# Kernel tuning notes

Hardware: AMD Instinct MI355X
Metric: run time of the kernel (lower is better)

Reference implementation:

```python
import jax, jax.numpy as jnp
import numpy as np

MAXDISP = 192  # must match init_kwargs max_disp


def _interp_axis(x, axis, out_size):
    """1-D linear interpolation along `axis` with align_corners=True."""
    in_size = x.shape[axis]
    src = jnp.arange(out_size, dtype=jnp.float32) * ((in_size - 1) / (out_size - 1))
    i0 = jnp.clip(jnp.floor(src).astype(jnp.int32), 0, in_size - 1)
    i1 = jnp.clip(i0 + 1, 0, in_size - 1)
    w = (src - i0.astype(jnp.float32)).astype(x.dtype)
    shape = [1] * x.ndim
    shape[axis] = out_size
    w = w.reshape(shape)
    return jnp.take(x, i0, axis=axis) * (1 - w) + jnp.take(x, i1, axis=axis) * w


def create_cost_volume(left, right, maxdisp):
    """Vectorized version of the original per-disparity slice-copy loop.
    cost[:, :C, d, :, w] = left[:, :, :, w]        if w >= d else 0
    cost[:, C:, d, :, w] = right[:, :, :, w - d]   if w >= d else 0
    Returns [B, 2C, D, H, W] with D = maxdisp // 4.
    """
    B, C, H, W = left.shape
    D = maxdisp // 4
    d = jnp.arange(D)[:, None]          # [D,1]
    w = jnp.arange(W)[None, :]          # [1,W]
    mask = (w >= d).astype(left.dtype)  # [D,W]
    idx = jnp.clip(w - d, 0, W - 1)     # [D,W] shifted gather indices
    mask_b = mask[None, None, :, None, :]                       # [1,1,D,1,W]
    cost_left = left[:, :, None, :, :] * mask_b                 # [B,C,D,H,W]
    cost_right = jnp.take(right, idx.reshape(-1), axis=3)       # [B,C,H,D*W]
    cost_right = cost_right.reshape(B, C, H, D, W)
    cost_right = jnp.transpose(cost_right, (0, 1, 3, 2, 4)) * mask_b
    return jnp.concatenate([cost_left, cost_right], axis=1)     # [B,2C,D,H,W]


def upsample_regression(vol, maxdisp):
    """Trilinear x4 upsample (align_corners=True) + softmax over disparity +
    soft-argmin expectation. vol: [B, D/4, H/4, W/4] -> [B, H, W]."""
    x = vol
    for axis in (1, 2, 3):
        x = _interp_axis(x, axis, x.shape[axis] * 4)
    p = jax.nn.softmax(x, axis=1)                       # [B, maxdisp, H, W]
    disps = jnp.arange(maxdisp, dtype=x.dtype)
    return jnp.einsum('bdhw,d->bhw', p, disps)


def setup_inputs() -> dict:
    key = jax.random.key(0)
    k1, k2 = jax.random.split(key)
    left = jax.random.normal(k1, (2, 32, 64, 128), dtype=jnp.float32)
    right = jax.random.normal(k2, (2, 32, 64, 128), dtype=jnp.float32)
    return {"left": left, "right": right}


def reference(left, right):
    cost = create_cost_volume(left, right, MAXDISP)  # [B,2C,D,H,W]
    # Stand-in for the (unavailable) stacked hourglass 3D-CNN: channel mean
    # reduces the cost volume to a single-channel disparity volume [B,D,H,W].
    vol = cost.mean(axis=1)
    return upsample_regression(vol, MAXDISP)  # [B, 4H, 4W]
```

## Files before the change

### kernel.cpp

```cpp
#include <hip/hip_runtime.h>

#define BB 2
#define CC 32
#define HC 64
#define WC 128
#define DC 48
#define HO 256
#define WO 512
#define MAXD 192

__global__ __launch_bounds__(256) void sum_channels_kernel(
    const float* __restrict__ left, const float* __restrict__ right,
    float* __restrict__ Ls, float* __restrict__ Rs) {
    __shared__ float sbuf[2][WC];
    int blk = blockIdx.x;
    int m   = blk >> 7;
    int b   = (blk >> 6) & 1;
    int h   = blk & (HC - 1);
    int t   = threadIdx.x;
    int sel = t >> 7;
    int w   = t & (WC - 1);

    const float* src = (m ? right : left)
                     + (size_t)b * (CC * HC * WC)
                     + (size_t)(sel * 16) * (HC * WC) + h * WC + w;
    float s = 0.f;
#pragma unroll
    for (int c = 0; c < 16; ++c) s += src[c * (HC * WC)];
    sbuf[sel][w] = s;
    __syncthreads();
    if (t < WC) {
        float* dst = m ? Rs : Ls;
        dst[b * (HC * WC) + h * WC + t] = sbuf[0][t] + sbuf[1][t];
    }
}

template <int K>
__device__ inline void quarter_work(const float* __restrict__ Rh,
                                    int w0, int w1, float c0, float c1,
                                    float lw0, float lw1,
                                    float& plsum, float& pssum) {
    constexpr int DDLO = 48 * K;
    constexpr int DDHI = 48 * K + 47;
    constexpr int DLO  = (DDLO * (DC - 1)) / (MAXD - 1);
    constexpr int DHI  = (DDHI * (DC - 1)) / (MAXD - 1);
    constexpr int NV   = DHI - DLO + 2;

    float vv[NV];
#pragma unroll
    for (int j = 0; j < NV; ++j) {
        int d = DLO + j;
        if (d > DC - 1) { vv[j] = vv[j - 1]; continue; }
        int i0 = w0 - d; float m0 = (i0 >= 0) ? 1.f : 0.f; i0 = max(i0, 0);
        int i1 = w1 - d; float m1 = (i1 >= 0) ? 1.f : 0.f; i1 = max(i1, 0);
        vv[j] = m0 * c0 * (lw0 + Rh[i0]) + m1 * c1 * (lw1 + Rh[i1]);
    }
    float ls = 0.f, ss = 0.f;
#pragma unroll
    for (int dd = DDLO; dd <= DDHI; ++dd) {
        int d    = (dd * (DC - 1)) / (MAXD - 1);
        float wd = (float)dd * (47.0f / 191.0f) - (float)d;
        float vc = vv[d - DLO];
        float x  = vc + wd * (vv[d - DLO + 1] - vc);
        float e  = __expf(x);
        ls += e;
        ss += e * (float)dd;
    }
    plsum = ls;
    pssum = ss;
}

__global__ __launch_bounds__(512) void disparity_kernel(
    const float* __restrict__ Ls, const float* __restrict__ Rs,
    float* __restrict__ out) {
    __shared__ float Lh[WC];
    __shared__ float Rh[WC];
    __shared__ float redL[4][WC];
    __shared__ float redS[4][WC];

    int blk = blockIdx.x;
    int r   = blk >> 2;
    int g   = blk & 3;
    int b   = r >> 8;
    int hh  = r & (HO - 1);

    float src_h = (float)hh * (63.0f / 255.0f);
    int h0 = (int)src_h; if (h0 > HC - 1) h0 = HC - 1;
    int h1 = min(h0 + 1, HC - 1);
    float fh = src_h - (float)h0;

    int t = threadIdx.x;

    if (t < WC) {
        const float* p = Ls + b * (HC * WC) + t;
        Lh[t] = (1.f - fh) * p[h0 * WC] + fh * p[h1 * WC];
    } else if (t < 2 * WC) {
        int u = t - WC;
        const float* p = Rs + b * (HC * WC) + u;
        Rh[u] = (1.f - fh) * p[h0 * WC] + fh * p[h1 * WC];
    }
    __syncthreads();

    int p = t & (WC - 1);
    int k = t >> 7;
    int ww = g * WC + p;

    float src_w = (float)ww * (127.0f / 511.0f);
    int w0 = (int)src_w; if (w0 > WC - 1) w0 = WC - 1;
    int w1 = min(w0 + 1, WC - 1);
    float fw = src_w - (float)w0;

    const float scale = 1.0f / 64.0f;
    float c0 = (1.f - fw) * scale;
    float c1 = fw * scale;
    float lw0 = Lh[w0];
    float lw1 = Lh[w1];

    float pls, pss;
    switch (k) {
        case 0: quarter_work<0>(Rh, w0, w1, c0, c1, lw0, lw1, pls, pss); break;
        case 1: quarter_work<1>(Rh, w0, w1, c0, c1, lw0, lw1, pls, pss); break;
        case 2: quarter_work<2>(Rh, w0, w1, c0, c1, lw0, lw1, pls, pss); break;
        default: quarter_work<3>(Rh, w0, w1, c0, c1, lw0, lw1, pls, pss); break;
    }
    redL[k][p] = pls;
    redS[k][p] = pss;
    __syncthreads();

    if (t < WC) {
        float ls = redL[0][t] + redL[1][t] + redL[2][t] + redL[3][t];
        float ss = redS[0][t] + redS[1][t] + redS[2][t] + redS[3][t];
        out[r * WO + g * WC + t] = ss / ls;
    }
}

extern "C" void kernel_launch(void* const* d_in, const int* in_sizes, int n_in,
                              void* d_out, int out_size, void* d_ws, size_t ws_size,
                              hipStream_t stream) {
    const float* left  = (const float*)d_in[0];
    const float* right = (const float*)d_in[1];
    float* out = (float*)d_out;
    float* Ls  = (float*)d_ws;
    float* Rs  = Ls + BB * HC * WC;

    sum_channels_kernel<<<256, 256, 0, stream>>>(left, right, Ls, Rs);
    disparity_kernel<<<BB * HO * 4, 512, 0, stream>>>(Ls, Rs, out);
}
```

Baseline: 70.15 us.

## Fuse channel sum into disparity kernel with incremental exp sweep per pixel

Merges the channel-sum kernel into the disparity kernel. Each block loads the two needed input rows with float4 reads and sums channels in shared memory, which drops one launch and the workspace round trip. Each thread now handles one output pixel across all 192 disparities. It uses exp2 with log2e folded into the coefficients, computes one exp per coarse segment, and steps with a multiplicative ratio in between. A zero-padded R buffer removes the per-element masking, and blocks are remapped for locality. The cost is redundant channel summation (each input row is re-read by several blocks), a longer serial chain per thread, and small numeric drift from the multiplicative exp stepping.

```diff
diff --git a/kernel.cpp b/kernel.cpp
--- a/kernel.cpp
+++ b/kernel.cpp
@@ -4,134 +4,130 @@
 #define CC 32
 #define HC 64
 #define WC 128
-#define DC 48
 #define HO 256
 #define WO 512
 #define MAXD 192
+#define NBLK (BB * HO)
+#define RPAD 47
+#define RSZ  176
 
-__global__ __launch_bounds__(256) void sum_channels_kernel(
-    const float* __restrict__ left, const float* __restrict__ right,
-    float* __restrict__ Ls, float* __restrict__ Rs) {
-    __shared__ float sbuf[2][WC];
-    int blk = blockIdx.x;
-    int m   = blk >> 7;
-    int b   = (blk >> 6) & 1;
-    int h   = blk & (HC - 1);
-    int t   = threadIdx.x;
-    int sel = t >> 7;
-    int w   = t & (WC - 1);
-
-    const float* src = (m ? right : left)
-                     + (size_t)b * (CC * HC * WC)
-                     + (size_t)(sel * 16) * (HC * WC) + h * WC + w;
-    float s = 0.f;
+template <bool MASKED>
+__device__ __forceinline__ float2 dd_sweep(const float* Rq,
+                                           float c0, float c1, float cA,
+                                           float cB0, float cB1, float fw0) {
+    const float KD = 47.0f / 191.0f;
+    float tc  = Rq[RPAD];
+    float tmm = Rq[RPAD + 1];
+    float vvc = fmaf(c0, tc, fmaf(c1, tmm, cA));
+    float tn = 0.f, vvn = 0.f, s = 0.f, e = 0.f, rr = 1.f;
+    float ls = 0.f, ss = 0.f;
 #pragma unroll
-    for (int c = 0; c < 16; ++c) s += src[c * (HC * WC)];
-    sbuf[sel][w] = s;
-    __syncthreads();
-    if (t < WC) {
-        float* dst = m ? Rs : Ls;
-        dst[b * (HC * WC) + h * WC + t] = sbuf[0][t] + sbuf[1][t];
+    for (int dd = 0; dd < MAXD; ++dd) {
+        const int d = (dd * 47) / 191;
+        const bool segstart = (dd == 0) || (d != (((dd - 1) * 47) / 191));
+        if (segstart) {
+            if (dd != 0) { vvc = vvn; tc = tn; }
+            if (d < 47) {
+                tn = Rq[RPAD - d - 1];
+                float bn;
+                if (MASKED) {
+                    float fd = (float)(d + 1);
+                    bn = fmaf(cB0, __saturatef(fw0 - fd + 1.f),
+                              cB1 * __saturatef(fw0 - fd + 2.f));
+                } else {
+                    bn = cA;
+                }
+                vvn = fmaf(c0, tn, fmaf(c1, tc, bn));
+                s = vvn - vvc;
+            } else {
+                s = 0.f;
+            }
+            const float wdf = (float)dd * KD - (float)d;
+            e  = __builtin_amdgcn_exp2f(fmaf(wdf, s, vvc));
+            rr = __builtin_amdgcn_exp2f(s * KD);
+        }
+        ls += e;
+        ss = fmaf(e, (float)dd, ss);
+        e *= rr;
     }
+    return make_float2(ls, ss);
 }
 
-template <int K>
-__device__ inline void quarter_work(const float* __restrict__ Rh,
-                                    int w0, int w1, float c0, float c1,
-                                    float lw0, float lw1,
-                                    float& plsum, float& pssum) {
-    constexpr int DDLO = 48 * K;
-    constexpr int DDHI = 48 * K + 47;
-    constexpr int DLO  = (DDLO * (DC - 1)) / (MAXD - 1);
-    constexpr int DHI  = (DDHI * (DC - 1)) / (MAXD - 1);
-    constexpr int NV   = DHI - DLO + 2;
-
-    float vv[NV];
-#pragma unroll
-    for (int j = 0; j < NV; ++j) {
-        int d = DLO + j;
-        if (d > DC - 1) { vv[j] = vv[j - 1]; continue; }
-        int i0 = w0 - d; float m0 = (i0 >= 0) ? 1.f : 0.f; i0 = max(i0, 0);
-        int i1 = w1 - d; float m1 = (i1 >= 0) ? 1.f : 0.f; i1 = max(i1, 0);
-        vv[j] = m0 * c0 * (lw0 + Rh[i0]) + m1 * c1 * (lw1 + Rh[i1]);
-    }
-    float ls = 0.f, ss = 0.f;
-#pragma unroll
-    for (int dd = DDLO; dd <= DDHI; ++dd) {
-        int d    = (dd * (DC - 1)) / (MAXD - 1);
-        float wd = (float)dd * (47.0f / 191.0f) - (float)d;
-        float vc = vv[d - DLO];
-        float x  = vc + wd * (vv[d - DLO + 1] - vc);
-        float e  = __expf(x);
-        ls += e;
-        ss += e * (float)dd;
-    }
-    plsum = ls;
-    pssum = ss;
-}
-
-__global__ __launch_bounds__(512) void disparity_kernel(
-    const float* __restrict__ Ls, const float* __restrict__ Rs,
+__global__ __launch_bounds__(512, 4) void fused_disp_kernel(
+    const float* __restrict__ left, const float* __restrict__ right,
     float* __restrict__ out) {
-    __shared__ float Lh[WC];
-    __shared__ float Rh[WC];
-    __shared__ float redL[4][WC];
-    __shared__ float redS[4][WC];
+    __shared__ float4 red[2][8][32];
+    __shared__ float  Lh[WC];
+    __shared__ float  Rhp[RSZ];
 
     int blk = blockIdx.x;
-    int r   = blk >> 2;
-    int g   = blk & 3;
+    int r   = (blk & 7) * (NBLK / 8) + (blk >> 3);
     int b   = r >> 8;
     int hh  = r & (HO - 1);
 
     float src_h = (float)hh * (63.0f / 255.0f);
     int h0 = (int)src_h; if (h0 > HC - 1) h0 = HC - 1;
-    int h1 = min(h0 + 1, HC - 1);
+    int h1 = h0 + 1;     if (h1 > HC - 1) h1 = HC - 1;
     float fh = src_h - (float)h0;
 
     int t = threadIdx.x;
 
-    if (t < WC) {
-        const float* p = Ls + b * (HC * WC) + t;
-        Lh[t] = (1.f - fh) * p[h0 * WC] + fh * p[h1 * WC];
-    } else if (t < 2 * WC) {
-        int u = t - WC;
-        const float* p = Rs + b * (HC * WC) + u;
-        Rh[u] = (1.f - fh) * p[h0 * WC] + fh * p[h1 * WC];
+    {
+        int mat = t >> 8;
+        int u   = t & 255;
+        int cg  = u >> 5;
+        int wq  = u & 31;
+        const float* srcp = (mat ? right : left) + (size_t)b * (CC * HC * WC);
+        float ax = 0.f, ay = 0.f, az = 0.f, aw = 0.f;
+        float bx = 0.f, by = 0.f, bz = 0.f, bw = 0.f;
+#pragma unroll
+        for (int i = 0; i < 4; ++i) {
+            int c = cg * 4 + i;
+            float4 v0 = *(const float4*)(srcp + ((c * HC + h0) * WC + wq * 4));
+            float4 v1 = *(const float4*)(srcp + ((c * HC + h1) * WC + wq * 4));
+            ax += v0.x; ay += v0.y; az += v0.z; aw += v0.w;
+            bx += v1.x; by += v1.y; bz += v1.z; bw += v1.w;
+        }
+        float gh = 1.f - fh;
+        red[mat][cg][wq] = make_float4(fmaf(gh, ax, fh * bx), fmaf(gh, ay, fh * by),
+                                       fmaf(gh, az, fh * bz), fmaf(gh, aw, fh * bw));
+    }
+    __syncthreads();
+    if (t < 256) {
+        int mat = t >> 7;
+        int w   = t & 127;
+        const float* redf = (const float*)red;
+        float s = 0.f;
+#pragma unroll
+        for (int cgi = 0; cgi < 8; ++cgi) s += redf[(mat * 8 + cgi) * 128 + w];
+        if (mat == 0) Lh[w] = s;
+        else          Rhp[RPAD + w] = s;
+    } else {
+        int z = t - 256;
+        if (z < RPAD)       Rhp[z] = 0.f;
+        else if (z == RPAD) Rhp[RSZ - 1] = 0.f;
     }
     __syncthreads();
 
-    int p = t & (WC - 1);
-    int k = t >> 7;
-    int ww = g * WC + p;
-
+    int ww = t;
     float src_w = (float)ww * (127.0f / 511.0f);
     int w0 = (int)src_w; if (w0 > WC - 1) w0 = WC - 1;
-    int w1 = min(w0 + 1, WC - 1);
+    int w1 = w0 + 1;     if (w1 > WC - 1) w1 = WC - 1;
     float fw = src_w - (float)w0;
 
-    const float scale = 1.0f / 64.0f;
-    float c0 = (1.f - fw) * scale;
-    float c1 = fw * scale;
-    float lw0 = Lh[w0];
-    float lw1 = Lh[w1];
+    const float L2E_SC = 1.4426950408889634f / 64.0f;
+    float c0  = (1.f - fw) * L2E_SC;
+    float c1  = fw * L2E_SC;
+    float lw0 = Lh[w0], lw1 = Lh[w1];
+    float cB0 = c0 * lw0, cB1 = c1 * lw1;
+    float cA  = cB0 + cB1;
+    float fw0 = (float)w0;
+    const float* Rq = Rhp + w0;
 
-    float pls, pss;
-    switch (k) {
-        case 0: quarter_work<0>(Rh, w0, w1, c0, c1, lw0, lw1, pls, pss); break;
-        case 1: quarter_work<1>(Rh, w0, w1, c0, c1, lw0, lw1, pls, pss); break;
-        case 2: quarter_work<2>(Rh, w0, w1, c0, c1, lw0, lw1, pls, pss); break;
-        default: quarter_work<3>(Rh, w0, w1, c0, c1, lw0, lw1, pls, pss); break;
-    }
-    redL[k][p] = pls;
-    redS[k][p] = pss;
-    __syncthreads();
+    float2 acc = (t < 192) ? dd_sweep<true >(Rq, c0, c1, cA, cB0, cB1, fw0)
+                           : dd_sweep<false>(Rq, c0, c1, cA, cB0, cB1, fw0);
 
-    if (t < WC) {
-        float ls = redL[0][t] + redL[1][t] + redL[2][t] + redL[3][t];
-        float ss = redS[0][t] + redS[1][t] + redS[2][t] + redS[3][t];
-        out[r * WO + g * WC + t] = ss / ls;
-    }
+    out[(size_t)(b * HO + hh) * WO + ww] = acc.y / acc.x;
 }
 
 extern "C" void kernel_launch(void* const* d_in, const int* in_sizes, int n_in,
@@ -139,10 +135,5 @@
                               hipStream_t stream) {
     const float* left  = (const float*)d_in[0];
     const float* right = (const float*)d_in[1];
-    float* out = (float*)d_out;
-    float* Ls  = (float*)d_ws;
-    float* Rs  = Ls + BB * HC * WC;
-
-    sum_channels_kernel<<<256, 256, 0, stream>>>(left, right, Ls, Rs);
-    disparity_kernel<<<BB * HO * 4, 512, 0, stream>>>(Ls, Rs, out);
+    fused_disp_kernel<<<NBLK, 512, 0, stream>>>(left, right, (float*)d_out);
 }
```

Result: slower. 127.6 us (+81.9%).
